# Performance work log

Hardware: AMD Instinct MI355X
Metric: run time of the kernel (lower is better)

## Reference

```python
import jax, jax.numpy as jnp
import numpy as np

B, N, K, LEN_INIT = 4, 4096, 10, 3
LEN_INPUT = 3 * (K + 1) + 3 * K + LEN_INIT  # 66


def setup_inputs() -> dict:
    key = jax.random.key(0)
    ks = jax.random.split(key, 6)
    return {
        "position": jax.random.normal(ks[0], (B, N, 3), dtype=jnp.float32),
        "velocity": jax.random.normal(ks[1], (B, N, 3), dtype=jnp.float32),
        "init_config": jax.random.normal(ks[2], (B, LEN_INIT), dtype=jnp.float32),
        "W1": jax.random.normal(ks[3], (32, LEN_INPUT), dtype=jnp.float32) * 0.1,
        "b1": jnp.zeros((32,), dtype=jnp.float32),
        "W2": jax.random.normal(ks[4], (16, 32), dtype=jnp.float32) * 0.1,
        "b2": jnp.zeros((16,), dtype=jnp.float32),
        "W3": jax.random.normal(ks[5], (6, 16), dtype=jnp.float32) * 0.1,
        "b3": jnp.zeros((6,), dtype=jnp.float32),
    }


def reference(position, velocity, init_config, W1, b1, W2, b2, W3, b3):
    Bc, Nc, _ = position.shape
    # pairwise squared distances [B,N,N]; same topk ordering as euclidean cdist
    sq = jnp.sum(position * position, axis=-1)  # [B,N]
    d2 = sq[:, :, None] + sq[:, None, :] - 2.0 * jnp.einsum("bnd,bmd->bnm", position, position)
    # k+1 nearest (including self), ascending distance
    _, nn_idx = jax.lax.top_k(-d2, K + 1)  # [B,N,K+1]
    # gather neighbor features per batch element
    vel_nn = jax.vmap(lambda v, i: v[i])(velocity, nn_idx)          # [B,N,K+1,3]
    pos_nn = jax.vmap(lambda p, i: p[i])(position, nn_idx[:, :, 1:])  # [B,N,K,3]
    pos_off = pos_nn - position[:, :, None, :]  # relative positions, no self
    feats = jnp.concatenate(
        [
            pos_off.reshape(Bc, Nc, 3 * K),
            vel_nn.reshape(Bc, Nc, 3 * (K + 1)),
            jnp.broadcast_to(init_config[:, None, :], (Bc, Nc, LEN_INIT)),
        ],
        axis=2,
    )  # [B,N,66]
    # three stacked linear layers (no nonlinearity, matching nn.Sequential of Linears)
    h = feats @ W1.T + b1
    h = h @ W2.T + b2
    pred = h @ W3.T + b3  # [B,N,6]
    return pred.at[:, :, :3].add(position)
```

## Files before the change

### kernel.cpp

```cpp
#include <hip/hip_runtime.h>
#include <stdint.h>

#define BATCH 4
#define NPTS 4096
#define KNN 11
#define LPQ 16
#define QPB 16
#define CHUNK 1024
#define NCHUNK (NPTS / CHUNK)
#define CPL (CHUNK / LPQ)
#define BUFN 10
#define SENT_BITS 0x433FFFFFFFFFFFFFll

__device__ __forceinline__ unsigned sortable_f32(float d) {
    unsigned b = __float_as_uint(d);
    unsigned m = (unsigned)(((int)b) >> 31) | 0x80000000u;
    return b ^ m;
}

__global__ __launch_bounds__(256)
__attribute__((amdgpu_waves_per_eu(4, 4))) void fused_kernel(
    const float* __restrict__ pos, const float* __restrict__ vel,
    const float* __restrict__ initc,
    const float* __restrict__ W1, const float* __restrict__ b1,
    const float* __restrict__ W2, const float* __restrict__ b2,
    const float* __restrict__ W3, const float* __restrict__ b3,
    float* __restrict__ out)
{
#pragma clang fp contract(off)
    __shared__ float4 sp[CHUNK + LPQ];
    __shared__ unsigned long long buf[BUFN * 256];

    int b    = blockIdx.x >> 8;
    int qblk = blockIdx.x & 255;
    int tid  = threadIdx.x;
    const float* pb = pos + (size_t)b * NPTS * 3;

    int q = tid >> 4, p = tid & 15;
    int i = qblk * QPB + q;

    float xq = pb[3*i], yq = pb[3*i+1], zq = pb[3*i+2];
    float sqq = xq*xq + yq*yq + zq*zq;

    double kd[KNN];
#pragma unroll
    for (int k = 0; k < KNN; ++k) kd[k] = __longlong_as_double(SENT_BITS);
    float tau_f = __builtin_inff();
    int cnt = 0, nflush = 0;

    for (int c = 0; c < NCHUNK; ++c) {
        if (c) __syncthreads();
        for (int j = tid; j < CHUNK; j += 256) {
            int g = c * CHUNK + j;
            float x = pb[3*g], y = pb[3*g+1], z = pb[3*g+2];
            float sq = x*x + y*y + z*z;
            sp[j + (j >> 6)] = make_float4(x, y, z, sq);
        }
        __syncthreads();

        int sbase = p * (CPL + 1);
        int jg    = c * CHUNK + p * CPL;
        for (int jl = 0; jl < CPL; jl += 4) {
            float4 c0 = sp[sbase + jl + 0];
            float4 c1 = sp[sbase + jl + 1];
            float4 c2 = sp[sbase + jl + 2];
            float4 c3 = sp[sbase + jl + 3];
            float t0 = xq*c0.x, t1 = xq*c1.x, t2 = xq*c2.x, t3 = xq*c3.x;
            t0 = fmaf(yq, c0.y, t0); t1 = fmaf(yq, c1.y, t1);
            t2 = fmaf(yq, c2.y, t2); t3 = fmaf(yq, c3.y, t3);
            t0 = fmaf(zq, c0.z, t0); t1 = fmaf(zq, c1.z, t1);
            t2 = fmaf(zq, c2.z, t2); t3 = fmaf(zq, c3.z, t3);
            float d0 = (sqq + c0.w) - 2.0f*t0;
            float d1 = (sqq + c1.w) - 2.0f*t1;
            float d2 = (sqq + c2.w) - 2.0f*t2;
            float d3 = (sqq + c3.w) - 2.0f*t3;

#pragma unroll
            for (int s = 0; s < 4; ++s) {
                float dv = s == 0 ? d0 : s == 1 ? d1 : s == 2 ? d2 : d3;
                if (dv <= tau_f) {
                    unsigned u  = sortable_f32(dv);
                    unsigned lo = (u << 12) | (unsigned)(jg + jl + s);
                    unsigned hi = 0x43300000u | (u >> 20);
                    buf[cnt * 256 + tid] =
                        ((unsigned long long)hi << 32) | (unsigned long long)lo;
                    ++cnt;
                }
            }

            if (__any(cnt > BUFN - 4)) {
                for (int k = 0; k < BUFN; ++k) {
                    if (!__any(cnt > k)) break;
                    unsigned long long kb = buf[k * 256 + tid];
                    double key = (k < cnt) ? __longlong_as_double(kb)
                                           : __longlong_as_double(SENT_BITS);
#pragma unroll
                    for (int kk = KNN-1; kk > 0; --kk) {
                        double mn = fmin(kd[kk], key);
                        kd[kk] = fmax(kd[kk-1], mn);
                    }
                    kd[0] = fmin(kd[0], key);
                }
                cnt = 0;
                if (nflush < 3) {
                    ++nflush;
                    double tmp[KNN];
#pragma unroll
                    for (int k = 0; k < KNN; ++k) tmp[k] = kd[k];
                    double h = tmp[0];
#pragma unroll
                    for (int r = 0; r < KNN; ++r) {
                        h = tmp[0];
#pragma unroll
                        for (int m = 1; m <= 8; m <<= 1)
                            h = fmin(h, __shfl_xor(h, m, LPQ));
                        bool own = (__double_as_longlong(tmp[0]) ==
                                    __double_as_longlong(h));
#pragma unroll
                        for (int t2 = 0; t2 < KNN-1; ++t2)
                            tmp[t2] = own ? tmp[t2+1] : tmp[t2];
                        tmp[KNN-1] = own ? __longlong_as_double(SENT_BITS)
                                         : tmp[KNN-1];
                    }
                    unsigned tau_u = (unsigned)((unsigned long long)
                                                __double_as_longlong(h) >> 12);
                    tau_f = __uint_as_float(tau_u ^ 0x80000000u);
                }
            }
        }
    }

    for (int k = 0; k < BUFN; ++k) {
        if (!__any(cnt > k)) break;
        unsigned long long kb = buf[k * 256 + tid];
        double key = (k < cnt) ? __longlong_as_double(kb)
                               : __longlong_as_double(SENT_BITS);
#pragma unroll
        for (int kk = KNN-1; kk > 0; --kk) {
            double mn = fmin(kd[kk], key);
            kd[kk] = fmax(kd[kk-1], mn);
        }
        kd[0] = fmin(kd[0], key);
    }

    unsigned res[KNN];
#pragma unroll
    for (int r = 0; r < KNN; ++r) {
        double h = kd[0];
#pragma unroll
        for (int m = 1; m <= 8; m <<= 1)
            h = fmin(h, __shfl_xor(h, m, LPQ));
        long long hb = __double_as_longlong(h);
        res[r] = (unsigned)(hb & 0xFFF);
        bool own = (__double_as_longlong(kd[0]) == hb);
#pragma unroll
        for (int t = 0; t < KNN-1; ++t) kd[t] = own ? kd[t+1] : kd[t];
        kd[KNN-1] = own ? __longlong_as_double(SENT_BITS) : kd[KNN-1];
    }

    const float* vb = vel + (size_t)b * NPTS * 3;

    const float* w0 = W1 + (2*p)   * 66;
    const float* w1 = W1 + (2*p+1) * 66;
    float a0 = b1[2*p], a1 = b1[2*p+1];
#pragma unroll
    for (int k = 1; k < KNN; ++k) {
        const float* pn = pb + 3*(int)res[k];
        float dx = pn[0] - xq, dy = pn[1] - yq, dz = pn[2] - zq;
        int ff = 3*(k-1);
        a0 = fmaf(dx, w0[ff+0], a0); a1 = fmaf(dx, w1[ff+0], a1);
        a0 = fmaf(dy, w0[ff+1], a0); a1 = fmaf(dy, w1[ff+1], a1);
        a0 = fmaf(dz, w0[ff+2], a0); a1 = fmaf(dz, w1[ff+2], a1);
    }
#pragma unroll
    for (int k = 0; k < KNN; ++k) {
        const float* vn = vb + 3*(int)res[k];
        int ff = 30 + 3*k;
        a0 = fmaf(vn[0], w0[ff+0], a0); a1 = fmaf(vn[0], w1[ff+0], a1);
        a0 = fmaf(vn[1], w0[ff+1], a0); a1 = fmaf(vn[1], w1[ff+1], a1);
        a0 = fmaf(vn[2], w0[ff+2], a0); a1 = fmaf(vn[2], w1[ff+2], a1);
    }
    float c0i = initc[b*3+0], c1i = initc[b*3+1], c2i = initc[b*3+2];
    a0 = fmaf(c0i, w0[63], a0); a1 = fmaf(c0i, w1[63], a1);
    a0 = fmaf(c1i, w0[64], a0); a1 = fmaf(c1i, w1[64], a1);
    a0 = fmaf(c2i, w0[65], a0); a1 = fmaf(c2i, w1[65], a1);

    float h2 = b2[p];
    const float* w2 = W2 + p * 32;
#pragma unroll
    for (int ii = 0; ii < 32; ++ii) {
        float h1v = __shfl((ii & 1) ? a1 : a0, ii >> 1, LPQ);
        h2 = fmaf(h1v, w2[ii], h2);
    }
    int o3 = p < 6 ? p : 0;
    float po = b3[o3];
    const float* w3 = W3 + o3 * 16;
#pragma unroll
    for (int ii = 0; ii < 16; ++ii) {
        float h2v = __shfl(h2, ii, LPQ);
        po = fmaf(h2v, w3[ii], po);
    }
    float resid = (p == 0) ? xq : (p == 1) ? yq : (p == 2) ? zq : 0.0f;
    po += resid;

    if (p < 6)
        out[((size_t)b * NPTS + (size_t)i) * 6 + p] = po;
}

extern "C" void kernel_launch(void* const* d_in, const int* in_sizes, int n_in,
                              void* d_out, int out_size, void* d_ws, size_t ws_size,
                              hipStream_t stream) {
    const float* pos   = (const float*)d_in[0];
    const float* vel   = (const float*)d_in[1];
    const float* initc = (const float*)d_in[2];
    const float* W1    = (const float*)d_in[3];
    const float* b1    = (const float*)d_in[4];
    const float* W2    = (const float*)d_in[5];
    const float* b2    = (const float*)d_in[6];
    const float* W3    = (const float*)d_in[7];
    const float* b3    = (const float*)d_in[8];
    float* out = (float*)d_out;

    fused_kernel<<<dim3(BATCH * (NPTS / QPB)), dim3(256), 0, stream>>>(
        pos, vel, initc, W1, b1, W2, b2, W3, b3, out);
}
```

Measured before the change: 125.4 us.

## Seed top-k threshold from per-lane minima of first 32 candidates

Before the main scan, each lane computes the minimum distance over its first 32 candidates in chunk 0. The lanes of a query then take the 11th smallest of those 16 minima by repeated shuffle-min and use it as the initial pruning threshold. This replaces the threshold refinement that ran over the first three buffer flushes. With a tight threshold from the start, fewer candidates should enter the buffer and fewer flushes should occur. The cost is an extra partial distance pass, and the seeded threshold is valid only if at least 11 distinct values exist, since equal minima across lanes are removed together.

```diff
diff --git a/kernel.cpp b/kernel.cpp
--- a/kernel.cpp
+++ b/kernel.cpp
@@ -46,7 +46,7 @@
 #pragma unroll
     for (int k = 0; k < KNN; ++k) kd[k] = __longlong_as_double(SENT_BITS);
     float tau_f = __builtin_inff();
-    int cnt = 0, nflush = 0;
+    int cnt = 0;
 
     for (int c = 0; c < NCHUNK; ++c) {
         if (c) __syncthreads();
@@ -60,6 +60,38 @@
 
         int sbase = p * (CPL + 1);
         int jg    = c * CHUNK + p * CPL;
+
+        if (c == 0) {
+            float mn = __builtin_inff();
+            for (int jl = 0; jl < 32; jl += 4) {
+                float4 c0 = sp[sbase + jl + 0];
+                float4 c1 = sp[sbase + jl + 1];
+                float4 c2 = sp[sbase + jl + 2];
+                float4 c3 = sp[sbase + jl + 3];
+                float t0 = xq*c0.x, t1 = xq*c1.x, t2 = xq*c2.x, t3 = xq*c3.x;
+                t0 = fmaf(yq, c0.y, t0); t1 = fmaf(yq, c1.y, t1);
+                t2 = fmaf(yq, c2.y, t2); t3 = fmaf(yq, c3.y, t3);
+                t0 = fmaf(zq, c0.z, t0); t1 = fmaf(zq, c1.z, t1);
+                t2 = fmaf(zq, c2.z, t2); t3 = fmaf(zq, c3.z, t3);
+                float d0 = (sqq + c0.w) - 2.0f*t0;
+                float d1 = (sqq + c1.w) - 2.0f*t1;
+                float d2 = (sqq + c2.w) - 2.0f*t2;
+                float d3 = (sqq + c3.w) - 2.0f*t3;
+                mn = fminf(mn, fminf(fminf(d0, d1), fminf(d2, d3)));
+            }
+            float mcur = mn, tau = mn;
+#pragma unroll
+            for (int r = 0; r < KNN; ++r) {
+                float h = mcur;
+#pragma unroll
+                for (int m = 1; m <= 8; m <<= 1)
+                    h = fminf(h, __shfl_xor(h, m, LPQ));
+                tau = h;
+                mcur = (mcur == h) ? __builtin_inff() : mcur;
+            }
+            tau_f = tau;
+        }
+
         for (int jl = 0; jl < CPL; jl += 4) {
             float4 c0 = sp[sbase + jl + 0];
             float4 c1 = sp[sbase + jl + 1];
@@ -96,36 +128,12 @@
                                            : __longlong_as_double(SENT_BITS);
 #pragma unroll
                     for (int kk = KNN-1; kk > 0; --kk) {
-                        double mn = fmin(kd[kk], key);
-                        kd[kk] = fmax(kd[kk-1], mn);
+                        double mn2 = fmin(kd[kk], key);
+                        kd[kk] = fmax(kd[kk-1], mn2);
                     }
                     kd[0] = fmin(kd[0], key);
                 }
                 cnt = 0;
-                if (nflush < 3) {
-                    ++nflush;
-                    double tmp[KNN];
-#pragma unroll
-                    for (int k = 0; k < KNN; ++k) tmp[k] = kd[k];
-                    double h = tmp[0];
-#pragma unroll
-                    for (int r = 0; r < KNN; ++r) {
-                        h = tmp[0];
-#pragma unroll
-                        for (int m = 1; m <= 8; m <<= 1)
-                            h = fmin(h, __shfl_xor(h, m, LPQ));
-                        bool own = (__double_as_longlong(tmp[0]) ==
-                                    __double_as_longlong(h));
-#pragma unroll
-                        for (int t2 = 0; t2 < KNN-1; ++t2)
-                            tmp[t2] = own ? tmp[t2+1] : tmp[t2];
-                        tmp[KNN-1] = own ? __longlong_as_double(SENT_BITS)
-                                         : tmp[KNN-1];
-                    }
-                    unsigned tau_u = (unsigned)((unsigned long long)
-                                                __double_as_longlong(h) >> 12);
-                    tau_f = __uint_as_float(tau_u ^ 0x80000000u);
-                }
             }
         }
     }
@@ -137,8 +145,8 @@
                                : __longlong_as_double(SENT_BITS);
 #pragma unroll
         for (int kk = KNN-1; kk > 0; --kk) {
-            double mn = fmin(kd[kk], key);
-            kd[kk] = fmax(kd[kk-1], mn);
+            double mn2 = fmin(kd[kk], key);
+            kd[kk] = fmax(kd[kk-1], mn2);
         }
         kd[0] = fmin(kd[0], key);
     }
```

Result: no change. 123.2 us (-1.8%).
